# Optimization experiments

Hardware: AMD Instinct MI355X
Metric: run time of the kernel (lower is better)

Reference implementation:

```python
import jax, jax.numpy as jnp
import numpy as np

EMBED_DIM = 1024
NUM_HEADS = 16
HEAD_DIM = EMBED_DIM // NUM_HEADS
ROPE_BASE = 10000.0


def setup_inputs() -> dict:
    key = jax.random.key(0)
    ks = jax.random.split(key, 9)
    B, S, E = 2, 2048, EMBED_DIM
    scale = 1.0 / np.sqrt(E)
    x = jax.random.normal(ks[0], (B, S, E), dtype=jnp.float32)
    Wq = jax.random.normal(ks[1], (E, E), dtype=jnp.float32) * scale
    bq = jnp.zeros((E,), dtype=jnp.float32)
    Wk = jax.random.normal(ks[2], (E, E), dtype=jnp.float32) * scale
    bk = jnp.zeros((E,), dtype=jnp.float32)
    Wv = jax.random.normal(ks[3], (E, E), dtype=jnp.float32) * scale
    bv = jnp.zeros((E,), dtype=jnp.float32)
    Wo = jax.random.normal(ks[4], (E, E), dtype=jnp.float32) * scale
    bo = jnp.zeros((E,), dtype=jnp.float32)
    return {"x": x, "Wq": Wq, "bq": bq, "Wk": Wk, "bk": bk,
            "Wv": Wv, "bv": bv, "Wo": Wo, "bo": bo}


def _rotary_emb(seq_len, dtype=jnp.float32):
    half = HEAD_DIM // 2
    inv_freq = 1.0 / (ROPE_BASE ** (jnp.arange(half, dtype=dtype) / half))
    pos = jnp.arange(seq_len, dtype=dtype)
    sinusoid = pos[:, None] * inv_freq[None, :]  # [S, half]
    sin = jnp.sin(sinusoid)
    cos = jnp.cos(sinusoid)
    # interleave-duplicate: (s0,s0,s1,s1,...) -> [S, HEAD_DIM]
    sin = jnp.stack((sin, sin), axis=-1).reshape(seq_len, HEAD_DIM)
    cos = jnp.stack((cos, cos), axis=-1).reshape(seq_len, HEAD_DIM)
    return sin, cos


def _rotate_half(x):
    x1 = x[..., ::2]
    x2 = x[..., 1::2]
    return jnp.stack((-x2, x1), axis=-1).reshape(x.shape)


def _apply_rope(x, sin, cos):
    # x: [B, H, S, D]; sin/cos: [S, D]
    return x * cos[None, None] + _rotate_half(x) * sin[None, None]


def reference(x, Wq, bq, Wk, bk, Wv, bv, Wo, bo):
    B, S, E = x.shape
    H, D = NUM_HEADS, HEAD_DIM

    def proj(W, b):
        t = x @ W.T + b  # [B, S, E]
        return t.reshape(B, S, H, D).transpose(0, 2, 1, 3)  # [B, H, S, D]

    q = proj(Wq, bq)
    k = proj(Wk, bk)
    v = proj(Wv, bv)

    sin, cos = _rotary_emb(S, x.dtype)
    q = _apply_rope(q, sin, cos)
    k = _apply_rope(k, sin, cos)

    scores = jnp.einsum("bhqd,bhkd->bhqk", q, k) / jnp.sqrt(jnp.asarray(D, x.dtype))
    causal = jnp.tril(jnp.ones((S, S), dtype=bool))  # keep lower triangle
    scores = jnp.where(causal[None, None], scores, -jnp.inf)
    weights = jax.nn.softmax(scores, axis=-1)
    out = jnp.einsum("bhqk,bhkd->bhqd", weights, v)
    out = out.transpose(0, 2, 1, 3).reshape(B, S, E)
    return out @ Wo.T + bo
```

## Files before the change

kernel.cpp:

```cpp
#include <hip/hip_runtime.h>
#include <hip/hip_bf16.h>
#include <cstdint>
#include <cstddef>

typedef __hip_bfloat16 bf16;
typedef __attribute__((ext_vector_type(8))) short bf16x8;
typedef __attribute__((ext_vector_type(4))) float f32x4;
typedef __attribute__((ext_vector_type(16))) float f32x16;

#define AS1C(p) ((const __attribute__((address_space(1))) void*)(p))
#define AS3(p)  ((__attribute__((address_space(3))) void*)(p))

constexpr int B_ = 2, S_ = 2048, E_ = 1024, H_ = 16, D_ = 64;
constexpr int M_ = B_ * S_;
constexpr float QSCALE_ = 0.125f * 1.44269504088896340736f;

__device__ __forceinline__ void gload_lds16(const bf16* g, bf16* l) {
  __builtin_amdgcn_global_load_lds(AS1C(g), AS3(l), 16, 0, 0);
}

__device__ __forceinline__ void cast4(const float* __restrict__ in, bf16* __restrict__ out, int i) {
  float4 v = reinterpret_cast<const float4*>(in)[i];
  union { bf16 b[4]; short4 s; } u;
  u.b[0] = __float2bfloat16(v.x);
  u.b[1] = __float2bfloat16(v.y);
  u.b[2] = __float2bfloat16(v.z);
  u.b[3] = __float2bfloat16(v.w);
  reinterpret_cast<short4*>(out)[i] = u.s;
}

__global__ void prep_kernel(const float* __restrict__ x,
                            const float* __restrict__ Wq, const float* __restrict__ Wk,
                            const float* __restrict__ Wv, const float* __restrict__ Wo,
                            const float* __restrict__ bq, const float* __restrict__ bk,
                            const float* __restrict__ bv,
                            bf16* __restrict__ xb, bf16* __restrict__ Wqkvb,
                            bf16* __restrict__ Wob, float* __restrict__ bqkv,
                            float* __restrict__ sintab, float* __restrict__ costab) {
  const int b = blockIdx.x, t = threadIdx.x;
  if (b < 4096) {
    cast4(x, xb, b * 256 + t);
  } else if (b < 5120) {
    cast4(Wo, Wob, (b - 4096) * 256 + t);
  } else if (b < 8192) {
    const int i = (b - 5120) * 256 + t;
    const int which = i >> 18;
    const int j = i & ((1 << 18) - 1);
    const float* src = which == 0 ? Wq : (which == 1 ? Wk : Wv);
    cast4(src, Wqkvb + (size_t)which * E_ * E_, j);
  } else if (b < 8448) {
    const int idx = (b - 8192) * 256 + t;
    const int s = idx >> 5, i = idx & 31;
    float inv = powf(10000.0f, -(float)i / 32.0f);
    float ang = (float)s * inv;
    sintab[idx] = sinf(ang);
    costab[idx] = cosf(ang);
  } else {
    for (int j = t; j < 768; j += 256) {
      const int which = j >> 8, jj = j & 255;
      const float* src = which == 0 ? bq : (which == 1 ? bk : bv);
      reinterpret_cast<float4*>(bqkv)[j] = reinterpret_cast<const float4*>(src)[jj];
    }
  }
}

__global__ __launch_bounds__(256)
void gemm_qkv(const bf16* __restrict__ A, const bf16* __restrict__ W,
              const float* __restrict__ bias,
              bf16* __restrict__ Qo, bf16* __restrict__ Ko, bf16* __restrict__ Vo,
              const float* __restrict__ sintab, const float* __restrict__ costab)
{
  constexpr int K = 1024, BK = 32;
  __shared__ __align__(16) bf16 smem[128 * 136];
  bf16* As = smem;
  bf16* Bs = smem + 128 * 32;
  const int tid = threadIdx.x;
  const int lane = tid & 63, wid = tid >> 6;
  const int g = lane >> 4, r16 = lane & 15;
  const int wr = wid >> 1, wc = wid & 1;
  const int swzr = (r16 >> 1) & 3;

  const int nwg = gridDim.x * gridDim.y;
  const int flat = blockIdx.y * gridDim.x + blockIdx.x;
  const int cpx = nwg >> 3;
  const int f2 = (flat & 7) * cpx + (flat >> 3);
  const int m0 = (f2 / gridDim.x) * 128, n0 = (f2 % gridDim.x) * 128;

  const f32x4 fz = {0.f, 0.f, 0.f, 0.f};
  f32x4 acc[4][4];
#pragma unroll
  for (int mi = 0; mi < 4; ++mi)
#pragma unroll
    for (int ni = 0; ni < 4; ++ni) acc[mi][ni] = fz;

  const bf16* Abase = A + (size_t)m0 * K;
  const bf16* Wbase = W + (size_t)n0 * K;
  const int c0 = tid, c1 = 256 + tid;
  const int r0c = c0 >> 2, cc0 = c0 & 3, sw0 = (r0c >> 1) & 3;
  const int r1c = c1 >> 2, cc1 = c1 & 3, sw1 = (r1c >> 1) & 3;

  for (int k0 = 0; k0 < K; k0 += BK) {
    __syncthreads();
    gload_lds16(Abase + (size_t)r0c * K + k0 + ((cc0 ^ sw0) * 8), As + c0 * 8);
    gload_lds16(Abase + (size_t)r1c * K + k0 + ((cc1 ^ sw1) * 8), As + c1 * 8);
    gload_lds16(Wbase + (size_t)r0c * K + k0 + ((cc0 ^ sw0) * 8), Bs + c0 * 8);
    gload_lds16(Wbase + (size_t)r1c * K + k0 + ((cc1 ^ sw1) * 8), Bs + c1 * 8);
    __syncthreads();

    bf16x8 af[4], bfr[4];
#pragma unroll
    for (int mi = 0; mi < 4; ++mi)
      af[mi] = *reinterpret_cast<const bf16x8*>(
          As + (wr * 64 + mi * 16 + r16) * BK + 8 * (g ^ swzr));
#pragma unroll
    for (int ni = 0; ni < 4; ++ni)
      bfr[ni] = *reinterpret_cast<const bf16x8*>(
          Bs + (wc * 64 + ni * 16 + r16) * BK + 8 * (g ^ swzr));
    __builtin_amdgcn_s_setprio(1);
#pragma unroll
    for (int mi = 0; mi < 4; ++mi)
#pragma unroll
      for (int ni = 0; ni < 4; ++ni)
        acc[mi][ni] = __builtin_amdgcn_mfma_f32_16x16x32_bf16(af[mi], bfr[ni], acc[mi][ni], 0, 0, 0);
    __builtin_amdgcn_s_setprio(0);
  }

  const int b = m0 >> 11;
  if (n0 >= 2048) {
    __syncthreads();
#pragma unroll
    for (int mi = 0; mi < 4; ++mi) {
#pragma unroll
      for (int ni = 0; ni < 4; ++ni) {
        const int n_local = wc * 64 + ni * 16 + r16;
        const float bv = bias[n0 + n_local];
        const int m_base = wr * 64 + mi * 16 + g * 4;
        union { bf16 b4[4]; short4 s4; } u;
#pragma unroll
        for (int r = 0; r < 4; ++r) u.b4[r] = __float2bfloat16(acc[mi][ni][r] + bv);
        *reinterpret_cast<short4*>(&smem[n_local * 136 + m_base]) = u.s4;
      }
    }
    __syncthreads();
    const int srow0 = m0 & (S_ - 1);
#pragma unroll
    for (int i = 0; i < 8; ++i) {
      const int c = i * 256 + tid;
      const int row = c >> 4, cc = c & 15;
      const bf16x8 v = *reinterpret_cast<const bf16x8*>(&smem[row * 136 + cc * 8]);
      const int n = n0 + row;
      const int h = (n >> 6) & 15, d = n & 63;
      *reinterpret_cast<bf16x8*>(&Vo[((size_t)(b * H_ + h) * D_ + d) * S_ + srow0 + cc * 8]) = v;
    }
  } else {
#pragma unroll
    for (int mi = 0; mi < 4; ++mi) {
#pragma unroll
      for (int ni = 0; ni < 4; ++ni) {
        const int gn = n0 + wc * 64 + ni * 16 + r16;
        const float bv = bias[gn];
#pragma unroll
        for (int r = 0; r < 4; ++r) {
          const int gm = m0 + wr * 64 + mi * 16 + g * 4 + r;
          float val = acc[mi][ni][r] + bv;
          const int d = gn & 63;
          const int srow = gm & (S_ - 1);
          const float cs = costab[srow * 32 + (d >> 1)];
          const float sn = sintab[srow * 32 + (d >> 1)];
          const float pv = __shfl_xor(val, 1);
          val = (d & 1) ? (val * cs + pv * sn) : (val * cs - pv * sn);
          const int h = (gn >> 6) & 15;
          const size_t bh = (size_t)(b * H_ + h);
          if (gn < 1024) {
            Qo[(bh * S_ + srow) * D_ + d] = __float2bfloat16(val * QSCALE_);
          } else {
            Ko[(bh * S_ + srow) * D_ + d] = __float2bfloat16(val);
          }
        }
      }
    }
  }
}

__global__ __launch_bounds__(256)
void gemm_o(const bf16* __restrict__ A, const bf16* __restrict__ W,
            const float* __restrict__ bias, float* __restrict__ outF)
{
  constexpr int K = 1024, BK = 32;
  __shared__ __align__(16) bf16 As[64 * BK];
  __shared__ __align__(16) bf16 Bs[128 * BK];
  const int tid = threadIdx.x;
  const int lane = tid & 63;
  const int wc = tid >> 6;
  const int g = lane >> 4, r16 = lane & 15;
  const int swzr = (r16 >> 1) & 3;

  const int flat = blockIdx.x;
  const int f2 = (flat & 7) * 64 + (flat >> 3);
  const int m0 = (f2 >> 3) * 64, n0 = (f2 & 7) * 128;

  const f32x4 fz = {0.f, 0.f, 0.f, 0.f};
  f32x4 acc[4][2];
#pragma unroll
  for (int mi = 0; mi < 4; ++mi)
#pragma unroll
    for (int ni = 0; ni < 2; ++ni) acc[mi][ni] = fz;

  const bf16* Abase = A + (size_t)m0 * K;
  const bf16* Wbase = W + (size_t)n0 * K;
  const int c0 = tid, c1 = 256 + tid;
  const int r0c = c0 >> 2, cc0 = c0 & 3, sw0 = (r0c >> 1) & 3;
  const int r1c = c1 >> 2, cc1 = c1 & 3, sw1 = (r1c >> 1) & 3;

  for (int k0 = 0; k0 < K; k0 += BK) {
    __syncthreads();
    gload_lds16(Abase + (size_t)r0c * K + k0 + ((cc0 ^ sw0) * 8), As + c0 * 8);
    gload_lds16(Wbase + (size_t)r0c * K + k0 + ((cc0 ^ sw0) * 8), Bs + c0 * 8);
    gload_lds16(Wbase + (size_t)r1c * K + k0 + ((cc1 ^ sw1) * 8), Bs + c1 * 8);
    __syncthreads();

    bf16x8 af[4], bfr[2];
#pragma unroll
    for (int mi = 0; mi < 4; ++mi)
      af[mi] = *reinterpret_cast<const bf16x8*>(
          As + (mi * 16 + r16) * BK + 8 * (g ^ swzr));
#pragma unroll
    for (int ni = 0; ni < 2; ++ni)
      bfr[ni] = *reinterpret_cast<const bf16x8*>(
          Bs + (wc * 32 + ni * 16 + r16) * BK + 8 * (g ^ swzr));
    __builtin_amdgcn_s_setprio(1);
#pragma unroll
    for (int mi = 0; mi < 4; ++mi)
#pragma unroll
      for (int ni = 0; ni < 2; ++ni)
        acc[mi][ni] = __builtin_amdgcn_mfma_f32_16x16x32_bf16(af[mi], bfr[ni], acc[mi][ni], 0, 0, 0);
    __builtin_amdgcn_s_setprio(0);
  }

#pragma unroll
  for (int mi = 0; mi < 4; ++mi)
#pragma unroll
    for (int ni = 0; ni < 2; ++ni) {
      const int gn = n0 + wc * 32 + ni * 16 + r16;
      const float bv = bias[gn];
#pragma unroll
      for (int r = 0; r < 4; ++r) {
        const int gm = m0 + mi * 16 + g * 4 + r;
        outF[(size_t)gm * 1024 + gn] = acc[mi][ni][r] + bv;
      }
    }
}

__global__ __launch_bounds__(256)
void attn_kernel(const bf16* __restrict__ Q, const bf16* __restrict__ Kg,
                 const bf16* __restrict__ Vtg, bf16* __restrict__ Og)
{
  __shared__ __align__(16) bf16 Ks[2][2][64 * 64];
  __shared__ __align__(16) bf16 Vs[2][2][64 * 64];
  const int flat = blockIdx.x;
  const int bh = flat & 31;
  const int qblk = 31 - (flat >> 5);
  const int tid = threadIdx.x, lane = tid & 63, wid = tid >> 6;
  const int qg = wid & 1, ksl = wid >> 1;
  const int l31 = lane & 31, h = lane >> 5;
  const bf16* Qb = Q + (size_t)bh * S_ * D_;
  const bf16* Kb = Kg + (size_t)bh * S_ * D_;
  const bf16* Vb = Vtg + (size_t)bh * D_ * S_;
  const int b = bh >> 4, hd = bh & 15;
  bf16* Ob = Og + (size_t)b * S_ * E_ + hd * D_;

  const int q0 = qblk * 64;
  const int qw0 = q0 + qg * 32;
  const int nkt = qblk + 1;
  const int nsup = (nkt + 1) >> 1;

  bf16x8 qf[4];
#pragma unroll
  for (int i = 0; i < 4; ++i)
    qf[i] = *reinterpret_cast<const bf16x8*>(Qb + (size_t)(qw0 + l31) * 64 + 16 * i + 8 * h);

  f32x16 oacc0 = {};
  f32x16 oacc1 = {};
  float mrow = -__builtin_inff();
  float lrow = 0.f;

  auto stagepair = [&](int jp, int dbuf) {
    const int t0 = 2 * jp;
#pragma unroll
    for (int i = 0; i < 4; ++i) {
      const int kc = tid + 256 * i;
      const int tile = kc >> 9, c2 = kc & 511, r = c2 >> 3, cc = c2 & 7;
      gload_lds16(Kb + (size_t)((t0 + tile) * 64 + r) * 64 + ((cc ^ (r & 7)) * 8),
                  &Ks[dbuf][tile][c2 * 8]);
    }
#pragma unroll
    for (int i = 0; i < 4; ++i) {
      const int kc = tid + 256 * i;
      const int tile = kc >> 9, c2 = kc & 511, r = c2 >> 3, cc = c2 & 7;
      gload_lds16(Vb + (size_t)r * S_ + (t0 + tile) * 64 + ((cc ^ (r & 7)) * 8),
                  &Vs[dbuf][tile][c2 * 8]);
    }
  };

  stagepair(0, 0);
  __syncthreads();
  int cur = 0;

  for (int j = 0; j < nsup; ++j) {
    if (j + 1 < nsup) stagepair(j + 1, cur ^ 1);

    const int kt = 2 * j + ksl;
    if (kt < nkt) {
      const int k0 = kt * 64;
      if (k0 <= qw0 + 31) {
        const bf16* ksp = Ks[cur][ksl];
        const bf16* vsp = Vs[cur][ksl];
        f32x16 ps0 = {}, ps1 = {};
        __builtin_amdgcn_s_setprio(1);
#pragma unroll
        for (int i = 0; i < 4; ++i) {
          const bf16x8 ka0 = *reinterpret_cast<const bf16x8*>(
              &ksp[l31 * 64 + (((2 * i + h) ^ (l31 & 7)) * 8)]);
          ps0 = __builtin_amdgcn_mfma_f32_32x32x16_bf16(ka0, qf[i], ps0, 0, 0, 0);
        }
#pragma unroll
        for (int i = 0; i < 4; ++i) {
          const int row1 = 32 + l31;
          const bf16x8 ka1 = *reinterpret_cast<const bf16x8*>(
              &ksp[row1 * 64 + (((2 * i + h) ^ (row1 & 7)) * 8)]);
          ps1 = __builtin_amdgcn_mfma_f32_32x32x16_bf16(ka1, qf[i], ps1, 0, 0, 0);
        }
        __builtin_amdgcn_s_setprio(0);
        if (k0 + 63 > qw0) {
          const int qm = qw0 + l31 - k0;
#pragma unroll
          for (int r = 0; r < 16; ++r) {
            const int kl = (r & 3) + 8 * (r >> 2) + 4 * h;
            if (kl > qm) ps0[r] = -1e30f;
            if (32 + kl > qm) ps1[r] = -1e30f;
          }
        }
        float tm = ps0[0];
#pragma unroll
        for (int r = 1; r < 16; ++r) tm = fmaxf(tm, ps0[r]);
#pragma unroll
        for (int r = 0; r < 16; ++r) tm = fmaxf(tm, ps1[r]);
        tm = fmaxf(tm, __shfl_xor(tm, 32));
        if (__any((tm - mrow > 8.f) ? 1 : 0)) {
          const float mn = fmaxf(mrow, tm);
          const float scl = exp2f(mrow - mn);
          mrow = mn;
          lrow *= scl;
          float so[16];
#pragma unroll
          for (int r = 0; r < 16; ++r)
            so[r] = __shfl(scl, (r & 3) + 8 * (r >> 2) + 4 * h);
#pragma unroll
          for (int r = 0; r < 16; ++r) { oacc0[r] *= so[r]; oacc1[r] *= so[r]; }
        }
        float ssum = 0.f;
#pragma unroll
        for (int r = 0; r < 16; ++r) {
          const float p = exp2f(ps0[r] - mrow);
          ps0[r] = p; ssum += p;
        }
#pragma unroll
        for (int r = 0; r < 16; ++r) {
          const float p = exp2f(ps1[r] - mrow);
          ps1[r] = p; ssum += p;
        }
        lrow += ssum;
        unsigned int pk0[8], pk1[8];
#pragma unroll
        for (int i = 0; i < 8; ++i) {
          unsigned int r0, r1;
          asm("v_cvt_pk_bf16_f32 %0, %1, %2" : "=v"(r0) : "v"(ps0[2 * i]), "v"(ps0[2 * i + 1]));
          asm("v_cvt_pk_bf16_f32 %0, %1, %2" : "=v"(r1) : "v"(ps1[2 * i]), "v"(ps1[2 * i + 1]));
          pk0[i] = r0; pk1[i] = r1;
        }
#pragma unroll
        for (int ks = 0; ks < 4; ++ks) {
          const int ksq = ks & 1;
          unsigned int w0, w1, w2, w3;
          if (ks < 2) { w0 = pk0[4 * ksq]; w2 = pk0[4 * ksq + 2];
                        w1 = pk0[4 * ksq + 1]; w3 = pk0[4 * ksq + 3]; }
          else        { w0 = pk1[4 * ksq]; w2 = pk1[4 * ksq + 2];
                        w1 = pk1[4 * ksq + 1]; w3 = pk1[4 * ksq + 3]; }
          asm("v_permlane32_swap_b32 %0, %1" : "+v"(w0), "+v"(w2));
          asm("v_permlane32_swap_b32 %0, %1" : "+v"(w1), "+v"(w3));
          union { unsigned int w[4]; bf16x8 v; } Aw;
          Aw.w[0] = w0; Aw.w[1] = w1; Aw.w[2] = w2; Aw.w[3] = w3;
          const int sw = l31 & 7;
          const bf16x8 vf0 = *reinterpret_cast<const bf16x8*>(
              &vsp[l31 * 64 + (((2 * ks + h) ^ sw) * 8)]);
          const bf16x8 vf1 = *reinterpret_cast<const bf16x8*>(
              &vsp[(32 + l31) * 64 + (((2 * ks + h) ^ sw) * 8)]);
          __builtin_amdgcn_s_setprio(1);
          oacc0 = __builtin_amdgcn_mfma_f32_32x32x16_bf16(Aw.v, vf0, oacc0, 0, 0, 0);
          oacc1 = __builtin_amdgcn_mfma_f32_32x32x16_bf16(Aw.v, vf1, oacc1, 0, 0, 0);
          __builtin_amdgcn_s_setprio(0);
        }
      }
    }

    __syncthreads();
    cur ^= 1;
  }

  lrow += __shfl_xor(lrow, 32);

  float* Obuf = (float*)&Ks[0][0][0];
  float* mlb  = (float*)&Vs[0][0][0];
  if (ksl == 1) {
#pragma unroll
    for (int r = 0; r < 16; ++r) {
      const int crow = (r & 3) + 8 * (r >> 2) + 4 * h;
      Obuf[(qg * 32 + crow) * 64 + l31] = oacc0[r];
      Obuf[(qg * 32 + crow) * 64 + 32 + l31] = oacc1[r];
    }
    if (h == 0) {
      mlb[(qg * 32 + l31) * 2] = mrow;
      mlb[(qg * 32 + l31) * 2 + 1] = lrow;
    }
  }
  __syncthreads();
  if (ksl == 0) {
    const float pm = mlb[(qg * 32 + l31) * 2];
    const float pl = mlb[(qg * 32 + l31) * 2 + 1];
    const float mstar = fmaxf(mrow, pm);
    const float a = exp2f(mrow - mstar);
    const float bb = exp2f(pm - mstar);
    const float linv = 1.0f / (lrow * a + pl * bb);
    const float fa = a * linv, fb = bb * linv;
#pragma unroll
    for (int r = 0; r < 16; ++r) {
      const int crow = (r & 3) + 8 * (r >> 2) + 4 * h;
      const float far = __shfl(fa, crow);
      const float fbr = __shfl(fb, crow);
      const int qrow = qw0 + crow;
      const float o0 = oacc0[r] * far + Obuf[(qg * 32 + crow) * 64 + l31] * fbr;
      const float o1 = oacc1[r] * far + Obuf[(qg * 32 + crow) * 64 + 32 + l31] * fbr;
      Ob[(size_t)qrow * E_ + l31] = __float2bfloat16(o0);
      Ob[(size_t)qrow * E_ + 32 + l31] = __float2bfloat16(o1);
    }
  }
}

extern "C" void kernel_launch(void* const* d_in, const int* in_sizes, int n_in,
                              void* d_out, int out_size, void* d_ws, size_t ws_size,
                              hipStream_t stream) {
  const float* x  = (const float*)d_in[0];
  const float* Wq = (const float*)d_in[1];
  const float* bq = (const float*)d_in[2];
  const float* Wk = (const float*)d_in[3];
  const float* bk = (const float*)d_in[4];
  const float* Wv = (const float*)d_in[5];
  const float* bv = (const float*)d_in[6];
  const float* Wo = (const float*)d_in[7];
  const float* bo = (const float*)d_in[8];
  float* out = (float*)d_out;

  char* ws = (char*)d_ws;
  size_t off = 0;
  auto alloc = [&](size_t bytes) -> char* {
    char* p = ws + off; off += (bytes + 255) & ~(size_t)255; return p;
  };
  bf16* xb    = (bf16*)alloc((size_t)M_ * E_ * 2);
  bf16* Wqkvb = (bf16*)alloc((size_t)3 * E_ * E_ * 2);
  bf16* Wob   = (bf16*)alloc((size_t)E_ * E_ * 2);
  float* bqkv = (float*)alloc((size_t)3 * E_ * 4);
  bf16* Qb    = (bf16*)alloc((size_t)M_ * E_ * 2);
  bf16* Kb    = (bf16*)alloc((size_t)M_ * E_ * 2);
  bf16* Vtb   = (bf16*)alloc((size_t)M_ * E_ * 2);
  bf16* AOb   = (bf16*)alloc((size_t)M_ * E_ * 2);
  float* sintab = (float*)alloc((size_t)S_ * 32 * 4);
  float* costab = (float*)alloc((size_t)S_ * 32 * 4);

  prep_kernel<<<dim3(8449), 256, 0, stream>>>(x, Wq, Wk, Wv, Wo, bq, bk, bv,
                                              xb, Wqkvb, Wob, bqkv, sintab, costab);

  gemm_qkv<<<dim3(24, 32), 256, 0, stream>>>(xb, Wqkvb, bqkv, Qb, Kb, Vtb, sintab, costab);
  attn_kernel<<<dim3(1024), 256, 0, stream>>>(Qb, Kb, Vtb, AOb);
  gemm_o<<<dim3(512), 256, 0, stream>>>(AOb, Wob, bo, out);
}
```

Measured before the change: 123.1 us.

## Double-buffer LDS tiles in QKV and output-projection GEMMs

Both projection GEMMs now keep two LDS tile buffers. The next K-slice is prefetched with global_load_lds into the alternate buffer while MFMAs consume the current one, which cuts the per-iteration barriers from two to one. This is meant to hide global-to-LDS load latency behind matrix compute, at the cost of doubled LDS for gemm_o. The QKV epilogue reuses the same shared array once the loop's final barrier has passed.

```diff
diff --git a/kernel.cpp b/kernel.cpp
--- a/kernel.cpp
+++ b/kernel.cpp
@@ -71,9 +71,7 @@
               const float* __restrict__ sintab, const float* __restrict__ costab)
 {
   constexpr int K = 1024, BK = 32;
-  __shared__ __align__(16) bf16 smem[128 * 136];
-  bf16* As = smem;
-  bf16* Bs = smem + 128 * 32;
+  __shared__ __align__(16) bf16 smem[17408];
   const int tid = threadIdx.x;
   const int lane = tid & 63, wid = tid >> 6;
   const int g = lane >> 4, r16 = lane & 15;
@@ -99,14 +97,24 @@
   const int r0c = c0 >> 2, cc0 = c0 & 3, sw0 = (r0c >> 1) & 3;
   const int r1c = c1 >> 2, cc1 = c1 & 3, sw1 = (r1c >> 1) & 3;
 
-  for (int k0 = 0; k0 < K; k0 += BK) {
-    __syncthreads();
+  auto stage = [&](int k0, int buf) {
+    bf16* As = smem + buf * 4096;
+    bf16* Bs = smem + 8192 + buf * 4096;
     gload_lds16(Abase + (size_t)r0c * K + k0 + ((cc0 ^ sw0) * 8), As + c0 * 8);
     gload_lds16(Abase + (size_t)r1c * K + k0 + ((cc1 ^ sw1) * 8), As + c1 * 8);
     gload_lds16(Wbase + (size_t)r0c * K + k0 + ((cc0 ^ sw0) * 8), Bs + c0 * 8);
     gload_lds16(Wbase + (size_t)r1c * K + k0 + ((cc1 ^ sw1) * 8), Bs + c1 * 8);
-    __syncthreads();
-
+  };
+
+  stage(0, 0);
+  __syncthreads();
+  int buf = 0;
+
+  for (int k0 = 0; k0 < K; k0 += BK) {
+    if (k0 + BK < K) stage(k0 + BK, buf ^ 1);
+
+    const bf16* As = smem + buf * 4096;
+    const bf16* Bs = smem + 8192 + buf * 4096;
     bf16x8 af[4], bfr[4];
 #pragma unroll
     for (int mi = 0; mi < 4; ++mi)
@@ -123,11 +131,13 @@
       for (int ni = 0; ni < 4; ++ni)
         acc[mi][ni] = __builtin_amdgcn_mfma_f32_16x16x32_bf16(af[mi], bfr[ni], acc[mi][ni], 0, 0, 0);
     __builtin_amdgcn_s_setprio(0);
+
+    __syncthreads();
+    buf ^= 1;
   }
 
   const int b = m0 >> 11;
   if (n0 >= 2048) {
-    __syncthreads();
 #pragma unroll
     for (int mi = 0; mi < 4; ++mi) {
 #pragma unroll
@@ -187,8 +197,8 @@
             const float* __restrict__ bias, float* __restrict__ outF)
 {
   constexpr int K = 1024, BK = 32;
-  __shared__ __align__(16) bf16 As[64 * BK];
-  __shared__ __align__(16) bf16 Bs[128 * BK];
+  __shared__ __align__(16) bf16 As[2][64 * BK];
+  __shared__ __align__(16) bf16 Bs[2][128 * BK];
   const int tid = threadIdx.x;
   const int lane = tid & 63;
   const int wc = tid >> 6;
@@ -212,22 +222,28 @@
   const int r0c = c0 >> 2, cc0 = c0 & 3, sw0 = (r0c >> 1) & 3;
   const int r1c = c1 >> 2, cc1 = c1 & 3, sw1 = (r1c >> 1) & 3;
 
+  auto stage = [&](int k0, int buf) {
+    gload_lds16(Abase + (size_t)r0c * K + k0 + ((cc0 ^ sw0) * 8), As[buf] + c0 * 8);
+    gload_lds16(Wbase + (size_t)r0c * K + k0 + ((cc0 ^ sw0) * 8), Bs[buf] + c0 * 8);
+    gload_lds16(Wbase + (size_t)r1c * K + k0 + ((cc1 ^ sw1) * 8), Bs[buf] + c1 * 8);
+  };
+
+  stage(0, 0);
+  __syncthreads();
+  int buf = 0;
+
   for (int k0 = 0; k0 < K; k0 += BK) {
-    __syncthreads();
-    gload_lds16(Abase + (size_t)r0c * K + k0 + ((cc0 ^ sw0) * 8), As + c0 * 8);
-    gload_lds16(Wbase + (size_t)r0c * K + k0 + ((cc0 ^ sw0) * 8), Bs + c0 * 8);
-    gload_lds16(Wbase + (size_t)r1c * K + k0 + ((cc1 ^ sw1) * 8), Bs + c1 * 8);
-    __syncthreads();
+    if (k0 + BK < K) stage(k0 + BK, buf ^ 1);
 
     bf16x8 af[4], bfr[2];
 #pragma unroll
     for (int mi = 0; mi < 4; ++mi)
       af[mi] = *reinterpret_cast<const bf16x8*>(
-          As + (mi * 16 + r16) * BK + 8 * (g ^ swzr));
+          As[buf] + (mi * 16 + r16) * BK + 8 * (g ^ swzr));
 #pragma unroll
     for (int ni = 0; ni < 2; ++ni)
       bfr[ni] = *reinterpret_cast<const bf16x8*>(
-          Bs + (wc * 32 + ni * 16 + r16) * BK + 8 * (g ^ swzr));
+          Bs[buf] + (wc * 32 + ni * 16 + r16) * BK + 8 * (g ^ swzr));
     __builtin_amdgcn_s_setprio(1);
 #pragma unroll
     for (int mi = 0; mi < 4; ++mi)
@@ -235,6 +251,9 @@
       for (int ni = 0; ni < 2; ++ni)
         acc[mi][ni] = __builtin_amdgcn_mfma_f32_16x16x32_bf16(af[mi], bfr[ni], acc[mi][ni], 0, 0, 0);
     __builtin_amdgcn_s_setprio(0);
+
+    __syncthreads();
+    buf ^= 1;
   }
 
 #pragma unroll
```

After: 114.3 us. -7.1%, faster.
